# Performance work log

Measured on AMD Instinct MI355X. Metric: run time of the kernel, lower is better.

Reference implementation:

```python
import jax, jax.numpy as jnp
import numpy as np
import math

N, E, D, R, L = 20000, 640000, 128, 16, 3
R_MAX = math.sqrt(2.0)
CENTERS = jnp.linspace(0.0, R_MAX, R)          # GaussianRBF centers on [0, sqrt(2)]
GAMMA = 1.0 / (2.0 * (R_MAX / (R - 1)) ** 2)   # 1/(2*sigma^2), sigma = center spacing


def _mlp(x, w1, b1, w2, b2):
    # mlp([din, d_h, dout]): Linear -> SiLU -> Linear (dropout=0.0)
    return jax.nn.silu(x @ w1 + b1) @ w2 + b2


def _ln(x, g, b):
    mu = jnp.mean(x, axis=-1, keepdims=True)
    v = jnp.var(x, axis=-1, keepdims=True)
    return (x - mu) * jax.lax.rsqrt(v + 1e-5) * g + b


def _time_emb(t):
    # SinusoidalEmbedding(dim=D)
    half = D // 2
    freqs = jnp.exp(-math.log(10000.0) * jnp.arange(half, dtype=jnp.float32) / (half - 1))
    a = t * freqs
    return jnp.concatenate([jnp.sin(a), jnp.cos(a)])


def setup_inputs():
    key = jax.random.key(0)
    ks = jax.random.split(key, 16)
    s = 0.05
    p = {}
    p["x_t"] = jax.random.normal(ks[0], (N, 3), dtype=jnp.float32)
    p["edge_index"] = jax.random.randint(ks[1], (2, E), 0, N)
    p["t"] = 25
    p["time_w1"] = jax.random.normal(ks[2], (D, D)) * s
    p["time_b1"] = jnp.zeros((D,))
    p["time_w2"] = jax.random.normal(ks[3], (D, D)) * s
    p["time_b2"] = jnp.zeros((D,))
    p["nodein_w1"] = jax.random.normal(ks[4], (3 + D, D)) * s
    p["nodein_b1"] = jnp.zeros((D,))
    p["nodein_w2"] = jax.random.normal(ks[5], (D, D)) * s
    p["nodein_b2"] = jnp.zeros((D,))
    p["phim_w1"] = jax.random.normal(ks[6], (L, 2 * D + R, D)) * s
    p["phim_b1"] = jnp.zeros((L, D))
    p["phim_w2"] = jax.random.normal(ks[7], (L, D, D)) * s
    p["phim_b2"] = jnp.zeros((L, D))
    p["phih_w1"] = jax.random.normal(ks[8], (L, 2 * D, D)) * s
    p["phih_b1"] = jnp.zeros((L, D))
    p["phih_w2"] = jax.random.normal(ks[9], (L, D, D)) * s
    p["phih_b2"] = jnp.zeros((L, D))
    p["ln_g"] = jnp.ones((L, D))
    p["ln_b"] = jnp.zeros((L, D))
    p["out_w1"] = jax.random.normal(ks[10], (D, D)) * s
    p["out_b1"] = jnp.zeros((D,))
    p["out_w2"] = jax.random.normal(ks[11], (D, 3)) * s
    p["out_b2"] = jnp.zeros((3,))
    return p


def reference(x_t, edge_index, t,
              time_w1, time_b1, time_w2, time_b2,
              nodein_w1, nodein_b1, nodein_w2, nodein_b2,
              phim_w1, phim_b1, phim_w2, phim_b2,
              phih_w1, phih_b1, phih_w2, phih_b2,
              ln_g, ln_b,
              out_w1, out_b1, out_w2, out_b2):
    # GraphDenoiser.forward: one denoiser call of the diffusion sampling loop.
    n = x_t.shape[0]
    src, dst = edge_index[0], edge_index[1]

    te = _mlp(_time_emb(jnp.asarray(t, jnp.float32)), time_w1, time_b1, time_w2, time_b2)
    h = _mlp(jnp.concatenate([x_t, jnp.broadcast_to(te, (n, D))], axis=-1),
             nodein_w1, nodein_b1, nodein_w2, nodein_b2)

    # edge geometry is fixed across layers (depends only on x_t)
    dx = x_t[src, :2] - x_t[dst, :2]                     # [E, 2]
    r = jnp.sqrt(jnp.sum(dx * dx, axis=-1) + 1e-8)       # [E]
    rbf = jnp.exp(-GAMMA * (r[:, None] - CENTERS) ** 2)  # [E, R]

    for i in range(L):  # WeightedInvariantMPNNLayer x L (edge_weight == 1)
        m_in = jnp.concatenate([h[src], h[dst], rbf], axis=-1)      # [E, 2D+R]
        m = _mlp(m_in, phim_w1[i], phim_b1[i], phim_w2[i], phim_b2[i])
        agg = jax.ops.segment_sum(m, dst, num_segments=n)           # scatter_sum
        h_up = _mlp(jnp.concatenate([h, agg], axis=-1),
                    phih_w1[i], phih_b1[i], phih_w2[i], phih_b2[i])
        h = _ln(h + h_up, ln_g[i], ln_b[i])

    return _mlp(h, out_w1, out_b1, out_w2, out_b2)  # predicted eps, [N, 3]
```

## Files before the change

kernel.cpp:

```cpp
#include <hip/hip_runtime.h>

typedef unsigned short u16;
typedef unsigned int u32;

#define NNODES 20000
#define NEDGES 640000
#define RBF_GAMMA 56.25f
#define SQRT2 1.4142135623730951f
#define PITCH 132
#define BPITCH 136

typedef __bf16 bf16x8 __attribute__((ext_vector_type(8)));
typedef __bf16 bf16x2 __attribute__((ext_vector_type(2)));
typedef float f32x4 __attribute__((ext_vector_type(4)));

__device__ __forceinline__ float b2f(u16 u) {
    union { float f; u32 i; } x; x.i = ((u32)u) << 16; return x.f;
}
__device__ __forceinline__ float hi2f(u32 w) {
    union { float f; u32 i; } x; x.i = w & 0xffff0000u; return x.f;
}
__device__ __forceinline__ float lo2f(u32 w) {
    union { float f; u32 i; } x; x.i = w << 16; return x.f;
}
__device__ __forceinline__ u16 f2b(float f) {
    union { float f; u32 i; } x; x.f = f;
    u32 r = (x.i + 0x7fffu + ((x.i >> 16) & 1u)) >> 16;
    return (u16)r;
}
__device__ __forceinline__ u32 pack2(float a, float b) {
#if __has_builtin(__builtin_amdgcn_cvt_pk_bf16_f32)
    union { bf16x2 v; u32 u; } x;
    x.v = __builtin_amdgcn_cvt_pk_bf16_f32(a, b);
    return x.u;
#else
    return (u32)f2b(a) | ((u32)f2b(b) << 16);
#endif
}
__device__ __forceinline__ float silu(float v) {
    return v * __builtin_amdgcn_rcpf(1.0f + __expf(-v));
}
__device__ __forceinline__ void fma4(float4 w, float4 s, float& acc) {
    acc = fmaf(w.x, s.x, acc);
    acc = fmaf(w.y, s.y, acc);
    acc = fmaf(w.z, s.z, acc);
    acc = fmaf(w.w, s.w, acc);
}

__global__ __launch_bounds__(256) void k_hist(const int* __restrict__ ei, int* __restrict__ hist) {
    int e = blockIdx.x * 256 + threadIdx.x;
    atomicAdd(&hist[ei[NEDGES + e]], 1);
}

__global__ __launch_bounds__(1024) void k_scan(const int* __restrict__ hist,
                                               int* __restrict__ row_ptr,
                                               int* __restrict__ cursor) {
    __shared__ int psum[1024];
    int t = threadIdx.x;
    int base = t * 20;
    int s = 0;
    if (base < NNODES)
        for (int i = 0; i < 20; ++i) s += hist[base + i];
    psum[t] = s;
    __syncthreads();
    for (int off = 1; off < 1024; off <<= 1) {
        int v = (t >= off) ? psum[t - off] : 0;
        __syncthreads();
        psum[t] += v;
        __syncthreads();
    }
    int excl = psum[t] - s;
    if (base < NNODES) {
        int run = excl;
        for (int i = 0; i < 20; ++i) {
            row_ptr[base + i] = run;
            cursor[base + i] = run;
            run += hist[base + i];
        }
    }
    if (t == 1023) row_ptr[NNODES] = psum[1023];
}

__global__ __launch_bounds__(256) void k_scatter(const int* __restrict__ ei, int* __restrict__ cursor,
                                                 int* __restrict__ ssrc, int* __restrict__ sdst) {
    int e = blockIdx.x * 256 + threadIdx.x;
    int d = ei[NEDGES + e];
    int pos = atomicAdd(&cursor[d], 1);
    ssrc[pos] = ei[e];
    sdst[pos] = d;
}

__global__ __launch_bounds__(256) void k_prep_wr(const float* __restrict__ pmw1,
                                                 const float* __restrict__ pmb1,
                                                 u16* __restrict__ Wr) {
    int id = blockIdx.x * 256 + threadIdx.x;
    if (id >= 1536) return;
    int l = id / 512; int r = id - l * 512;
    int nt = r >> 6, lane = r & 63;
    int col = nt * 16 + (lane & 15);
    alignas(16) u16 tmp[8];
    #pragma unroll
    for (int jj = 0; jj < 8; ++jj) {
        int kk = (lane >> 4) * 8 + jj;
        float v = 0.f;
        if (kk < 16) v = pmw1[l * 34816 + (256 + kk) * 128 + col];
        else if (kk == 16) v = pmb1[l * 128 + col];
        tmp[jj] = f2b(v);
    }
    *(uint4*)(Wr + (size_t)id * 8) = *(const uint4*)tmp;
}

struct BfM { const float* s[10]; };
__global__ __launch_bounds__(256) void k_prep_bf(BfM bf, u16* __restrict__ dst) {
    int id = blockIdx.x * 256 + threadIdx.x;
    if (id >= 20480) return;
    int mat = id >> 11;
    int r = id & 2047;
    int kc = r >> 9;
    int r2 = r & 511;
    int nt = r2 >> 6, lane = r2 & 63;
    int col = nt * 16 + (lane & 15);
    int kb = kc * 32 + (lane >> 4) * 8;
    const float* src = bf.s[mat];
    alignas(16) u16 tmp[8];
    #pragma unroll
    for (int jj = 0; jj < 8; ++jj)
        tmp[jj] = f2b(src[(kb + jj) * 128 + col]);
    *(uint4*)(dst + (size_t)id * 8) = *(const uint4*)tmp;
}

struct PackM { const float* s[4]; float* d[4]; int K[4]; };
__global__ __launch_bounds__(256) void k_pack(PackM pm) {
    int m = blockIdx.y;
    int idx = blockIdx.x * 256 + threadIdx.x;
    if (idx >= pm.K[m] * 128) return;
    int k = idx >> 7, j = idx & 127;
    pm.d[m][(k >> 2) * 512 + j * 4 + (k & 3)] = pm.s[m][idx];
}

__global__ __launch_bounds__(256) void k_prep_m(const float* __restrict__ pmw2,
        const float* __restrict__ pmb2, const float* __restrict__ V1p,
        float* __restrict__ Mp, float* __restrict__ bvv) {
    const int l = blockIdx.y, bx = blockIdx.x;
    const float* V1 = V1p + (size_t)l * 32768;
    const int tid = threadIdx.x;
    const int w = tid >> 6, lane = tid & 63;
    const int cg = lane & 15, ng = lane >> 4;
    const int jc0 = w * 32 + cg * 2, jc1 = jc0 + 1;
    __shared__ alignas(16) float W2L[16][PITCH];
    __shared__ float b2L[128];
    if (bx < 8) {
        const float4* src = (const float4*)(pmw2 + (size_t)l * 16384 + bx * 16 * 128);
        for (int q = tid; q < 512; q += 256) {
            int row = q >> 5, part = q & 31;
            *(float4*)&W2L[row][part * 4] = src[q];
        }
        __syncthreads();
        int r0 = ng * 4;
        float acc[4][2];
        #pragma unroll
        for (int n = 0; n < 4; ++n) { acc[n][0] = 0.f; acc[n][1] = 0.f; }
        for (int mm = 0; mm < 32; ++mm) {
            float4 wa = *(const float4*)(V1 + (32 + mm) * 512 + jc0 * 4);
            float4 wb = *(const float4*)(V1 + (32 + mm) * 512 + jc1 * 4);
            #pragma unroll
            for (int n = 0; n < 4; ++n) {
                float4 s4 = *(const float4*)&W2L[r0 + n][mm * 4];
                fma4(wa, s4, acc[n][0]);
                fma4(wb, s4, acc[n][1]);
            }
        }
        #pragma unroll
        for (int n = 0; n < 4; ++n) {
            int kg = bx * 16 + r0 + n;
            Mp[(size_t)l * 16384 + (kg >> 2) * 512 + jc0 * 4 + (kg & 3)] = acc[n][0];
            Mp[(size_t)l * 16384 + (kg >> 2) * 512 + jc1 * 4 + (kg & 3)] = acc[n][1];
        }
    } else {
        if (tid < 128) b2L[tid] = pmb2[l * 128 + tid];
        __syncthreads();
        if (ng == 0) {
            float a0 = 0.f, a1 = 0.f;
            for (int mm = 0; mm < 32; ++mm) {
                float4 wa = *(const float4*)(V1 + (32 + mm) * 512 + jc0 * 4);
                float4 wb = *(const float4*)(V1 + (32 + mm) * 512 + jc1 * 4);
                float4 s4 = *(const float4*)&b2L[mm * 4];
                fma4(wa, s4, a0);
                fma4(wb, s4, a1);
            }
            bvv[l * 128 + jc0] = a0;
            bvv[l * 128 + jc1] = a1;
        }
    }
}

__global__ __launch_bounds__(128) void k_time(const int* __restrict__ tptr,
        const float* __restrict__ tw1, const float* __restrict__ tb1,
        const float* __restrict__ tw2, const float* __restrict__ tb2,
        const float* __restrict__ nw1, const float* __restrict__ nb1,
        float* __restrict__ base1) {
    __shared__ float emb[128], hid[128], te[128];
    int j = threadIdx.x;
    int raw = tptr[0];
    float tv;
    if (raw >= 0 && raw < (1 << 24)) tv = (float)raw;
    else tv = __int_as_float(raw);
    float fr = expf(-9.210340371976184f * (float)(j & 63) / 63.0f);
    float a = tv * fr;
    emb[j] = (j < 64) ? sinf(a) : cosf(a);
    __syncthreads();
    float acc = tb1[j];
    for (int k = 0; k < 128; ++k) acc += emb[k] * tw1[k * 128 + j];
    hid[j] = silu(acc);
    __syncthreads();
    acc = tb2[j];
    for (int k = 0; k < 128; ++k) acc += hid[k] * tw2[k * 128 + j];
    te[j] = acc;
    __syncthreads();
    acc = nb1[j];
    for (int k = 0; k < 128; ++k) acc += te[k] * nw1[(3 + k) * 128 + j];
    base1[j] = acc;
}

__global__ __launch_bounds__(256) void k_h0(const float* __restrict__ x, const float* __restrict__ base1,
        const float* __restrict__ nw1, const float* __restrict__ nw2p, const float* __restrict__ nb2,
        const u16* __restrict__ Yw,
        float* __restrict__ hf, u16* __restrict__ Ysrc, u16* __restrict__ Ydst) {
    const int tid = threadIdx.x;
    const int w = tid >> 6, lane = tid & 63;
    const int cg = lane & 15, ng = lane >> 4;
    const int jc0 = w * 32 + cg * 2, jc1 = jc0 + 1;
    const int n0 = ng * 4;
    const int base = blockIdx.x * 16;
    __shared__ alignas(16) float xl[16][4];
    __shared__ alignas(16) float hid[16][PITCH];
    __shared__ alignas(16) u16 hb16[16 * BPITCH];
    if (tid < 48) { int n = tid / 3, cc = tid - n * 3; xl[n][cc] = x[(size_t)(base + n) * 3 + cc]; }
    __syncthreads();
    {
        float w0a = nw1[jc0], w0b = nw1[jc1];
        float w1a = nw1[128 + jc0], w1b = nw1[128 + jc1];
        float w2a = nw1[256 + jc0], w2b = nw1[256 + jc1];
        float ba = base1[jc0], bb = base1[jc1];
        #pragma unroll
        for (int n = 0; n < 4; ++n) {
            int row = n0 + n;
            float x0 = xl[row][0], x1 = xl[row][1], x2 = xl[row][2];
            float2 v;
            v.x = silu(ba + x0 * w0a + x1 * w1a + x2 * w2a);
            v.y = silu(bb + x0 * w0b + x1 * w1b + x2 * w2b);
            *(float2*)&hid[row][jc0] = v;
        }
    }
    __syncthreads();
    float acc[4][2];
    {
        float ba = nb2[jc0], bb = nb2[jc1];
        #pragma unroll
        for (int n = 0; n < 4; ++n) { acc[n][0] = ba; acc[n][1] = bb; }
        for (int kk = 0; kk < 32; ++kk) {
            float4 wa = *(const float4*)(nw2p + kk * 512 + jc0 * 4);
            float4 wb = *(const float4*)(nw2p + kk * 512 + jc1 * 4);
            #pragma unroll
            for (int n = 0; n < 4; ++n) {
                float4 s4 = *(const float4*)&hid[n0 + n][kk * 4];
                fma4(wa, s4, acc[n][0]);
                fma4(wb, s4, acc[n][1]);
            }
        }
    }
    __syncthreads();
    #pragma unroll
    for (int n = 0; n < 4; ++n) {
        int row = n0 + n;
        *(float2*)&hf[(size_t)(base + row) * 128 + jc0] = make_float2(acc[n][0], acc[n][1]);
        *(u32*)&hb16[row * BPITCH + jc0] = pack2(acc[n][0], acc[n][1]);
    }
    __syncthreads();
    {
        const int mat = w >> 1, half = w & 1;
        const int lrow = lane & 15, quad = lane >> 4;
        bf16x8 a[4];
        #pragma unroll
        for (int kc = 0; kc < 4; ++kc)
            a[kc] = *(const bf16x8*)(hb16 + lrow * BPITCH + kc * 32 + quad * 8);
        u16* dst = mat ? Ydst : Ysrc;
        #pragma unroll
        for (int t = 0; t < 4; ++t) {
            int nt = half * 4 + t;
            f32x4 a4 = {0.f, 0.f, 0.f, 0.f};
            #pragma unroll
            for (int kc = 0; kc < 4; ++kc) {
                bf16x8 b = *(const bf16x8*)(Yw + (size_t)(((mat * 4 + kc) * 8 + nt) * 512 + lane * 8));
                a4 = __builtin_amdgcn_mfma_f32_16x16x32_bf16(a[kc], b, a4, 0, 0, 0);
            }
            #pragma unroll
            for (int r = 0; r < 4; ++r)
                dst[(size_t)(base + quad * 4 + r) * 128 + nt * 16 + lrow] = f2b(a4[r]);
        }
    }
}

__global__ __launch_bounds__(512, 8) void k_edge(
        const u16* __restrict__ Ysrc, const u16* __restrict__ Ydst,
        const float* __restrict__ x,
        const int* __restrict__ ssrc, const int* __restrict__ sdst,
        const u16* __restrict__ Wr,
        float* __restrict__ s_glob) {
    __shared__ alignas(16) u16 sst[128 * 72];
    __shared__ alignas(16) u16 ys[64 * 128];
    __shared__ float rv[64];
    __shared__ int s_d[65];
    __shared__ int s_s[64];
    const int tid = threadIdx.x;
    const int e0 = blockIdx.x * 64;
    if (tid < 64) {
        int s = ssrc[e0 + tid], d = sdst[e0 + tid];
        s_s[tid] = s; s_d[tid] = d;
        float ddx = x[s * 3] - x[d * 3];
        float ddy = x[s * 3 + 1] - x[d * 3 + 1];
        rv[tid] = sqrtf(ddx * ddx + ddy * ddy + 1e-8f);
    } else if (tid == 64) {
        s_d[64] = -1;
    }
    __syncthreads();
    #pragma unroll
    for (int i = 0; i < 2; ++i) {
        int cch = tid + i * 512;
        int e = cch >> 4, part = cch & 15;
        *(uint4*)(ys + e * 128 + part * 8) = *(const uint4*)(Ysrc + (size_t)s_s[e] * 128 + part * 8);
    }
    const int w = tid >> 6, lane = tid & 63;
    const int m = w & 3, nh = w >> 2;
    const int lrow = lane & 15, quad = lane >> 4;
    float r = rv[m * 16 + lrow];
    union { bf16x8 v; u16 u[8]; } af;
    #pragma unroll
    for (int j = 0; j < 8; ++j) {
        int kk = quad * 8 + j;
        float v;
        if (kk < 16) {
            float dd = r - SQRT2 * (float)kk / 15.0f;
            v = __expf(-RBF_GAMMA * dd * dd);
        } else v = (kk == 16) ? 1.0f : 0.0f;
        af.u[j] = f2b(v);
    }
    {
        const u16* Bp = Wr + lane * 8;
        #pragma unroll
        for (int t = 0; t < 4; ++t) {
            int nt = nh * 4 + t;
            f32x4 a4 = {0.f, 0.f, 0.f, 0.f};
            bf16x8 b = *(const bf16x8*)(Bp + nt * 512);
            a4 = __builtin_amdgcn_mfma_f32_16x16x32_bf16(af.v, b, a4, 0, 0, 0);
            int col = nt * 16 + lrow;
            u32 lo = pack2(a4[0], a4[1]);
            u32 hi = pack2(a4[2], a4[3]);
            *(uint2*)(sst + col * 72 + m * 16 + quad * 4) = make_uint2(lo, hi);
        }
    }
    __syncthreads();
    {
        const int col = tid & 127, q = tid >> 7;
        const int r0 = q * 16;
        float a = 0.f;
        int cd = s_d[r0];
        float yd = b2f(Ydst[(size_t)cd * 128 + col]);
        #pragma unroll
        for (int h = 0; h < 2; ++h) {
            uint4 c0 = *(const uint4*)(sst + col * 72 + r0 + h * 8);
            float sv8[8];
            sv8[0] = lo2f(c0.x); sv8[1] = hi2f(c0.x);
            sv8[2] = lo2f(c0.y); sv8[3] = hi2f(c0.y);
            sv8[4] = lo2f(c0.z); sv8[5] = hi2f(c0.z);
            sv8[6] = lo2f(c0.w); sv8[7] = hi2f(c0.w);
            #pragma unroll
            for (int i = 0; i < 8; ++i) {
                int rr = r0 + h * 8 + i;
                int nd = s_d[rr + 1];
                float v = sv8[i] + b2f(ys[rr * 128 + col]) + yd;
                a += silu(v);
                bool last = (h == 1 && i == 7);
                if (last || nd != cd) {
                    atomicAdd(&s_glob[(size_t)cd * 128 + col], a);
                    a = 0.f;
                    if (!last && nd != cd)
                        yd = b2f(Ydst[(size_t)nd * 128 + col]);
                }
                cd = nd;
            }
        }
    }
}

__global__ __launch_bounds__(256) void k_node(float* __restrict__ s_glob, const int* __restrict__ row_ptr,
        float* __restrict__ hf,
        const float* __restrict__ Mp, const float* __restrict__ V1p, const u16* __restrict__ V2bf,
        const float* __restrict__ bv, const float* __restrict__ c1, const float* __restrict__ c2,
        const float* __restrict__ lng, const float* __restrict__ lnb,
        const u16* __restrict__ Yw,
        u16* __restrict__ Ysrc, u16* __restrict__ Ydst) {
    const int tid = threadIdx.x;
    const int w = tid >> 6, lane = tid & 63;
    const int cg = lane & 15, ng = lane >> 4;
    const int jc0 = w * 32 + cg * 2, jc1 = jc0 + 1;
    const int n0 = ng * 4;
    const int base = blockIdx.x * 16;
    const int lrow = lane & 15, quad = lane >> 4;
    __shared__ alignas(16) float sv[16][PITCH], hv[16][PITCH];
    __shared__ alignas(16) u16 ybf[16 * BPITCH];
    __shared__ float mv[16][2];
    __shared__ int rp[17];
    float (*xs)[PITCH] = sv;

    if (tid < 17) rp[tid] = row_ptr[base + tid];
    {
        const float4* sg4 = (const float4*)(s_glob + (size_t)base * 128);
        float4* sg4w = (float4*)(s_glob + (size_t)base * 128);
        const float4* hg4 = (const float4*)(hf + (size_t)base * 128);
        for (int q = tid; q < 512; q += 256) {
            int row = q >> 5, part = q & 31;
            *(float4*)&sv[row][part * 4] = sg4[q];
            *(float4*)&hv[row][part * 4] = hg4[q];
            sg4w[q] = make_float4(0.f, 0.f, 0.f, 0.f);
        }
    }
    __syncthreads();

    float acc[4][2];
    {
        float ba = c1[jc0], bb = c1[jc1];
        float bva = bv[jc0], bvb = bv[jc1];
        #pragma unroll
        for (int n = 0; n < 4; ++n) {
            float dg = (float)(rp[n0 + n + 1] - rp[n0 + n]);
            acc[n][0] = ba + dg * bva; acc[n][1] = bb + dg * bvb;
        }
        for (int kk = 0; kk < 32; ++kk) {
            float4 wa = *(const float4*)(V1p + kk * 512 + jc0 * 4);
            float4 wb = *(const float4*)(V1p + kk * 512 + jc1 * 4);
            #pragma unroll
            for (int n = 0; n < 4; ++n) {
                float4 s4 = *(const float4*)&hv[n0 + n][kk * 4];
                fma4(wa, s4, acc[n][0]);
                fma4(wb, s4, acc[n][1]);
            }
        }
        for (int kk = 0; kk < 32; ++kk) {
            float4 wa = *(const float4*)(Mp + kk * 512 + jc0 * 4);
            float4 wb = *(const float4*)(Mp + kk * 512 + jc1 * 4);
            #pragma unroll
            for (int n = 0; n < 4; ++n) {
                float4 s4 = *(const float4*)&sv[n0 + n][kk * 4];
                fma4(wa, s4, acc[n][0]);
                fma4(wb, s4, acc[n][1]);
            }
        }
        #pragma unroll
        for (int n = 0; n < 4; ++n)
            *(u32*)&ybf[(n0 + n) * BPITCH + jc0] = pack2(silu(acc[n][0]), silu(acc[n][1]));
    }
    __syncthreads();
    {
        bf16x8 a[4];
        #pragma unroll
        for (int kc = 0; kc < 4; ++kc)
            a[kc] = *(const bf16x8*)(ybf + lrow * BPITCH + kc * 32 + quad * 8);
        #pragma unroll
        for (int t = 0; t < 2; ++t) {
            int nt = w * 2 + t;
            f32x4 a4 = {0.f, 0.f, 0.f, 0.f};
            #pragma unroll
            for (int kc = 0; kc < 4; ++kc) {
                bf16x8 b = *(const bf16x8*)(V2bf + (size_t)((kc * 8 + nt) * 512 + lane * 8));
                a4 = __builtin_amdgcn_mfma_f32_16x16x32_bf16(a[kc], b, a4, 0, 0, 0);
            }
            int colC = nt * 16 + lrow;
            float c2v = c2[colC];
            #pragma unroll
            for (int r = 0; r < 4; ++r) {
                int R = quad * 4 + r;
                xs[R][colC] = a4[r] + c2v + hv[R][colC];
            }
        }
    }
    __syncthreads();
    {
        int row = tid >> 4, part = tid & 15;
        float4 a = *(const float4*)&xs[row][part * 8];
        float4 b = *(const float4*)&xs[row][part * 8 + 4];
        float s1 = a.x + a.y + a.z + a.w + b.x + b.y + b.z + b.w;
        float s2 = a.x * a.x + a.y * a.y + a.z * a.z + a.w * a.w
                 + b.x * b.x + b.y * b.y + b.z * b.z + b.w * b.w;
        #pragma unroll
        for (int mq = 1; mq < 16; mq <<= 1) {
            s1 += __shfl_xor(s1, mq, 64);
            s2 += __shfl_xor(s2, mq, 64);
        }
        if (part == 0) { mv[row][0] = s1; mv[row][1] = s2; }
    }
    __syncthreads();
    {
        float ga = lng[jc0], gb = lng[jc1];
        float bba = lnb[jc0], bbb = lnb[jc1];
        #pragma unroll
        for (int n = 0; n < 4; ++n) {
            int row = n0 + n;
            float mu = mv[row][0] * (1.0f / 128.0f);
            float var = mv[row][1] * (1.0f / 128.0f) - mu * mu;
            float rs = rsqrtf(var + 1e-5f);
            float y0 = (xs[row][jc0] - mu) * rs * ga + bba;
            float y1 = (xs[row][jc1] - mu) * rs * gb + bbb;
            *(float2*)&hf[(size_t)(base + row) * 128 + jc0] = make_float2(y0, y1);
            *(u32*)&ybf[row * BPITCH + jc0] = pack2(y0, y1);
        }
    }
    if (Yw != nullptr) {
        __syncthreads();
        const int mat = w >> 1, half = w & 1;
        bf16x8 a[4];
        #pragma unroll
        for (int kc = 0; kc < 4; ++kc)
            a[kc] = *(const bf16x8*)(ybf + lrow * BPITCH + kc * 32 + quad * 8);
        u16* dst = mat ? Ydst : Ysrc;
        #pragma unroll
        for (int t = 0; t < 4; ++t) {
            int nt = half * 4 + t;
            f32x4 a4 = {0.f, 0.f, 0.f, 0.f};
            #pragma unroll
            for (int kc = 0; kc < 4; ++kc) {
                bf16x8 b = *(const bf16x8*)(Yw + (size_t)(((mat * 4 + kc) * 8 + nt) * 512 + lane * 8));
                a4 = __builtin_amdgcn_mfma_f32_16x16x32_bf16(a[kc], b, a4, 0, 0, 0);
            }
            #pragma unroll
            for (int r = 0; r < 4; ++r)
                dst[(size_t)(base + quad * 4 + r) * 128 + nt * 16 + lrow] = f2b(a4[r]);
        }
    }
}

__global__ __launch_bounds__(256) void k_out(const float* __restrict__ hf, const u16* __restrict__ ow1bf,
        const float* __restrict__ ob1, const float* __restrict__ ow2, const float* __restrict__ ob2,
        float* __restrict__ out) {
    const int tid = threadIdx.x;
    const int w = tid >> 6, lane = tid & 63;
    const int lrow = lane & 15, quad = lane >> 4;
    const int base = blockIdx.x * 16;
    __shared__ alignas(16) u16 hb16[16 * BPITCH];
    __shared__ float hid[16][PITCH];
    for (int q = tid; q < 512; q += 256) {
        int row = q >> 5, part = q & 31;
        float4 v = ((const float4*)(hf + (size_t)base * 128))[q];
        *(uint2*)&hb16[row * BPITCH + part * 4] = make_uint2(pack2(v.x, v.y), pack2(v.z, v.w));
    }
    __syncthreads();
    {
        bf16x8 a[4];
        #pragma unroll
        for (int kc = 0; kc < 4; ++kc)
            a[kc] = *(const bf16x8*)(hb16 + lrow * BPITCH + kc * 32 + quad * 8);
        #pragma unroll
        for (int t = 0; t < 2; ++t) {
            int nt = w * 2 + t;
            f32x4 a4 = {0.f, 0.f, 0.f, 0.f};
            #pragma unroll
            for (int kc = 0; kc < 4; ++kc) {
                bf16x8 b = *(const bf16x8*)(ow1bf + (size_t)((kc * 8 + nt) * 512 + lane * 8));
                a4 = __builtin_amdgcn_mfma_f32_16x16x32_bf16(a[kc], b, a4, 0, 0, 0);
            }
            int colC = nt * 16 + lrow;
            float b1v = ob1[colC];
            #pragma unroll
            for (int r = 0; r < 4; ++r)
                hid[quad * 4 + r][colC] = silu(a4[r] + b1v);
        }
    }
    __syncthreads();
    if (tid < 48) {
        int n = tid / 3, cc = tid - n * 3;
        float o = ob2[cc];
        for (int k = 0; k < 128; ++k) o += hid[n][k] * ow2[k * 3 + cc];
        out[(size_t)(base + n) * 3 + cc] = o;
    }
}

extern "C" void kernel_launch(void* const* d_in, const int* in_sizes, int n_in,
                              void* d_out, int out_size, void* d_ws, size_t ws_size,
                              hipStream_t stream) {
    const float* x    = (const float*)d_in[0];
    const int* ei     = (const int*)d_in[1];
    const int* tptr   = (const int*)d_in[2];
    const float* tw1  = (const float*)d_in[3];
    const float* tb1  = (const float*)d_in[4];
    const float* tw2  = (const float*)d_in[5];
    const float* tb2  = (const float*)d_in[6];
    const float* nw1  = (const float*)d_in[7];
    const float* nb1  = (const float*)d_in[8];
    const float* nw2  = (const float*)d_in[9];
    const float* nb2  = (const float*)d_in[10];
    const float* pmw1 = (const float*)d_in[11];
    const float* pmb1 = (const float*)d_in[12];
    const float* pmw2 = (const float*)d_in[13];
    const float* pmb2 = (const float*)d_in[14];
    const float* phw1 = (const float*)d_in[15];
    const float* phb1 = (const float*)d_in[16];
    const float* phw2 = (const float*)d_in[17];
    const float* phb2 = (const float*)d_in[18];
    const float* lng  = (const float*)d_in[19];
    const float* lnb  = (const float*)d_in[20];
    const float* ow1  = (const float*)d_in[21];
    const float* ob1  = (const float*)d_in[22];
    const float* ow2  = (const float*)d_in[23];
    const float* ob2  = (const float*)d_in[24];
    float* out = (float*)d_out;

    char* wsp = (char*)d_ws;
    size_t off = 0;
    auto alloc = [&](size_t bytes) -> void* {
        void* p = wsp + off;
        off += (bytes + 255) & ~(size_t)255;
        return p;
    };
    int* hist    = (int*)alloc((size_t)NNODES * 4);
    int* cursor  = (int*)alloc((size_t)NNODES * 4);
    int* row_ptr = (int*)alloc((size_t)(NNODES + 1) * 4);
    int* ssrc    = (int*)alloc((size_t)NEDGES * 4);
    int* sdst    = (int*)alloc((size_t)NEDGES * 4);
    u16* Wr      = (u16*)alloc((size_t)3 * 8 * 64 * 8 * 2);
    u16* BF      = (u16*)alloc((size_t)10 * 16384 * 2);
    float* base1 = (float*)alloc(128 * 4);
    float* V1p   = (float*)alloc((size_t)3 * 256 * 128 * 4);
    float* nw2p  = (float*)alloc((size_t)128 * 128 * 4);
    float* Mp    = (float*)alloc((size_t)3 * 128 * 128 * 4);
    float* bvv   = (float*)alloc((size_t)3 * 128 * 4);
    float* hf    = (float*)alloc((size_t)NNODES * 128 * 4);
    u16* Ysrc    = (u16*)alloc((size_t)NNODES * 128 * 2);
    u16* Ydst    = (u16*)alloc((size_t)NNODES * 128 * 2);
    float* s_glob= (float*)alloc((size_t)NNODES * 128 * 4);

    (void)hipMemsetAsync(hist, 0, (size_t)NNODES * 4, stream);
    k_hist<<<NEDGES / 256, 256, 0, stream>>>(ei, hist);
    k_scan<<<1, 1024, 0, stream>>>(hist, row_ptr, cursor);
    k_scatter<<<NEDGES / 256, 256, 0, stream>>>(ei, cursor, ssrc, sdst);
    k_prep_wr<<<6, 256, 0, stream>>>(pmw1, pmb1, Wr);

    BfM bf;
    for (int l = 0; l < 3; ++l) {
        bf.s[l * 2 + 0] = pmw1 + (size_t)l * 34816;
        bf.s[l * 2 + 1] = pmw1 + (size_t)l * 34816 + 16384;
        bf.s[6 + l] = phw2 + (size_t)l * 16384;
    }
    bf.s[9] = ow1;
    k_prep_bf<<<80, 256, 0, stream>>>(bf, BF);

    PackM pm;
    for (int l = 0; l < 3; ++l) {
        pm.s[l] = phw1 + (size_t)l * 32768; pm.d[l] = V1p + (size_t)l * 32768; pm.K[l] = 256;
    }
    pm.s[3] = nw2; pm.d[3] = nw2p; pm.K[3] = 128;
    k_pack<<<dim3(128, 4), 256, 0, stream>>>(pm);
    k_prep_m<<<dim3(9, 3), 256, 0, stream>>>(pmw2, pmb2, V1p, Mp, bvv);

    k_time<<<1, 128, 0, stream>>>(tptr, tw1, tb1, tw2, tb2, nw1, nb1, base1);
    k_h0<<<1250, 256, 0, stream>>>(x, base1, nw1, nw2p, nb2, BF, hf, Ysrc, Ydst);

    (void)hipMemsetAsync(s_glob, 0, (size_t)NNODES * 128 * 4, stream);
    for (int l = 0; l < 3; ++l) {
        k_edge<<<NEDGES / 64, 512, 0, stream>>>(Ysrc, Ydst, x, ssrc, sdst,
                Wr + (size_t)l * 4096, s_glob);
        const u16* YwN = (l < 2) ? (BF + (size_t)(l + 1) * 32768) : nullptr;
        k_node<<<1250, 256, 0, stream>>>(s_glob, row_ptr, hf,
                Mp + (size_t)l * 16384, V1p + (size_t)l * 32768, BF + (size_t)(6 + l) * 16384,
                bvv + l * 128, phb1 + l * 128, phb2 + l * 128, lng + l * 128, lnb + l * 128,
                YwN, Ysrc, Ydst);
    }
    k_out<<<1250, 256, 0, stream>>>(hf, BF + (size_t)9 * 16384, ob1, ow2, ob2, out);
}
```

Before: 535.0 us.

## Restructure edge epilogue with per-block destination slots and staged Ydst rows

The edge kernel now groups consecutive equal destinations into slots using a wave ballot, prefetches up to 16 unique destination rows of Ydst into shared memory, and stores the RBF projection row-major. Each thread now handles two columns across 8 edges with paired u32 loads instead of one column across 16 edges. Together these aim to cut scattered global Ydst loads and shared-memory access cost. Segments are shorter, so more atomics may be issued, and slots beyond 16 fall back to global loads.

```diff
diff --git a/kernel.cpp b/kernel.cpp
--- a/kernel.cpp
+++ b/kernel.cpp
@@ -307,21 +307,29 @@
         const int* __restrict__ ssrc, const int* __restrict__ sdst,
         const u16* __restrict__ Wr,
         float* __restrict__ s_glob) {
-    __shared__ alignas(16) u16 sst[128 * 72];
+    __shared__ alignas(16) u16 sst[64 * 136];
     __shared__ alignas(16) u16 ys[64 * 128];
+    __shared__ alignas(16) u16 ydl[16 * 128];
     __shared__ float rv[64];
-    __shared__ int s_d[65];
     __shared__ int s_s[64];
+    __shared__ int s_slot[64];
+    __shared__ int dstmap[64];
+    __shared__ int s_ns;
     const int tid = threadIdx.x;
     const int e0 = blockIdx.x * 64;
     if (tid < 64) {
         int s = ssrc[e0 + tid], d = sdst[e0 + tid];
-        s_s[tid] = s; s_d[tid] = d;
+        s_s[tid] = s;
         float ddx = x[s * 3] - x[d * 3];
         float ddy = x[s * 3 + 1] - x[d * 3 + 1];
         rv[tid] = sqrtf(ddx * ddx + ddy * ddy + 1e-8f);
-    } else if (tid == 64) {
-        s_d[64] = -1;
+        int dprev = __shfl_up(d, 1, 64);
+        bool flag = (tid == 0) || (d != dprev);
+        unsigned long long bm = __ballot(flag);
+        int slot = __popcll(bm & ((2ull << tid) - 1)) - 1;
+        s_slot[tid] = slot;
+        if (flag) dstmap[slot] = d;
+        if (tid == 0) s_ns = __popcll(bm);
     }
     __syncthreads();
     #pragma unroll
@@ -329,6 +337,14 @@
         int cch = tid + i * 512;
         int e = cch >> 4, part = cch & 15;
         *(uint4*)(ys + e * 128 + part * 8) = *(const uint4*)(Ysrc + (size_t)s_s[e] * 128 + part * 8);
+    }
+    {
+        int nsc = s_ns < 16 ? s_ns : 16;
+        for (int idx = tid; idx < nsc * 64; idx += 512) {
+            int row = idx >> 6, part = idx & 63;
+            *(u32*)(ydl + row * 128 + part * 2) =
+                *(const u32*)(Ydst + (size_t)dstmap[row] * 128 + part * 2);
+        }
     }
     const int w = tid >> 6, lane = tid & 63;
     const int m = w & 3, nh = w >> 2;
@@ -347,49 +363,54 @@
     }
     {
         const u16* Bp = Wr + lane * 8;
+        const int row0 = m * 16 + quad * 4;
         #pragma unroll
         for (int t = 0; t < 4; ++t) {
             int nt = nh * 4 + t;
             f32x4 a4 = {0.f, 0.f, 0.f, 0.f};
             bf16x8 b = *(const bf16x8*)(Bp + nt * 512);
             a4 = __builtin_amdgcn_mfma_f32_16x16x32_bf16(af.v, b, a4, 0, 0, 0);
-            int col = nt * 16 + lrow;
-            u32 lo = pack2(a4[0], a4[1]);
-            u32 hi = pack2(a4[2], a4[3]);
-            *(uint2*)(sst + col * 72 + m * 16 + quad * 4) = make_uint2(lo, hi);
-        }
-    }
-    __syncthreads();
-    {
-        const int col = tid & 127, q = tid >> 7;
-        const int r0 = q * 16;
-        float a = 0.f;
-        int cd = s_d[r0];
-        float yd = b2f(Ydst[(size_t)cd * 128 + col]);
-        #pragma unroll
-        for (int h = 0; h < 2; ++h) {
-            uint4 c0 = *(const uint4*)(sst + col * 72 + r0 + h * 8);
-            float sv8[8];
-            sv8[0] = lo2f(c0.x); sv8[1] = hi2f(c0.x);
-            sv8[2] = lo2f(c0.y); sv8[3] = hi2f(c0.y);
-            sv8[4] = lo2f(c0.z); sv8[5] = hi2f(c0.z);
-            sv8[6] = lo2f(c0.w); sv8[7] = hi2f(c0.w);
-            #pragma unroll
-            for (int i = 0; i < 8; ++i) {
-                int rr = r0 + h * 8 + i;
-                int nd = s_d[rr + 1];
-                float v = sv8[i] + b2f(ys[rr * 128 + col]) + yd;
-                a += silu(v);
-                bool last = (h == 1 && i == 7);
-                if (last || nd != cd) {
-                    atomicAdd(&s_glob[(size_t)cd * 128 + col], a);
-                    a = 0.f;
-                    if (!last && nd != cd)
-                        yd = b2f(Ydst[(size_t)nd * 128 + col]);
-                }
-                cd = nd;
-            }
-        }
+            int colw = nt * 16 + lrow;
+            #pragma unroll
+            for (int rr = 0; rr < 4; ++rr)
+                sst[(row0 + rr) * 136 + colw] = f2b(a4[rr]);
+        }
+    }
+    __syncthreads();
+    {
+        const int cp = tid & 63;
+        const int oct = tid >> 6;
+        const int eb = oct * 8;
+        int cur = s_slot[eb];
+        u32 ydw = (cur < 16) ? *(const u32*)(ydl + cur * 128 + cp * 2)
+                             : *(const u32*)(Ydst + (size_t)dstmap[cur] * 128 + cp * 2);
+        float yd0 = lo2f(ydw), yd1 = hi2f(ydw);
+        float a0 = 0.f, a1 = 0.f;
+        float* sg = s_glob + 2 * cp;
+        #pragma unroll
+        for (int i = 0; i < 8; ++i) {
+            int rr = eb + i;
+            int sl = s_slot[rr];
+            if (sl != cur) {
+                float* p = sg + (size_t)dstmap[cur] * 128;
+                atomicAdd(p, a0);
+                atomicAdd(p + 1, a1);
+                a0 = 0.f; a1 = 0.f;
+                ydw = (sl < 16) ? *(const u32*)(ydl + sl * 128 + cp * 2)
+                                : *(const u32*)(Ydst + (size_t)dstmap[sl] * 128 + cp * 2);
+                yd0 = lo2f(ydw); yd1 = hi2f(ydw);
+                cur = sl;
+            }
+            u32 sw = *(const u32*)(sst + rr * 136 + cp * 2);
+            u32 yw = *(const u32*)(ys + rr * 128 + cp * 2);
+            float v0 = lo2f(sw) + lo2f(yw) + yd0;
+            float v1 = hi2f(sw) + hi2f(yw) + yd1;
+            a0 = fmaf(v0, __builtin_amdgcn_rcpf(1.0f + __expf(-v0)), a0);
+            a1 = fmaf(v1, __builtin_amdgcn_rcpf(1.0f + __expf(-v1)), a1);
+        }
+        float* p = sg + (size_t)dstmap[cur] * 128;
+        atomicAdd(p, a0);
+        atomicAdd(p + 1, a1);
     }
 }
 
```

After: 611.6 us. 1.14x slower.
